# Optimization experiments

Hardware: AMD Instinct MI355X
Metric: run time of the kernel (lower is better)

Reference implementation:

```python
import jax, jax.numpy as jnp
import numpy as np

D_MODEL = 1024
N_HEADS = 16
D_K = D_MODEL // N_HEADS
B, T = 4, 2048


def setup_inputs() -> dict:
    key = jax.random.key(0)
    ks = jax.random.split(key, 13)
    s = 1.0 / np.sqrt(D_MODEL)
    inp = {
        "Q": jax.random.normal(ks[0], (B, T, D_MODEL), jnp.float32),
        "K": jax.random.normal(ks[1], (B, T, D_MODEL), jnp.float32),
        "V": jax.random.normal(ks[2], (B, T, D_MODEL), jnp.float32),
        "mask": jax.random.randint(ks[3], (B, 1, 1, T), 0, 2, jnp.int32),
        "W_q": jax.random.normal(ks[4], (D_MODEL, D_MODEL), jnp.float32) * s,
        "b_q": jax.random.normal(ks[5], (D_MODEL,), jnp.float32) * s,
        "W_k": jax.random.normal(ks[6], (D_MODEL, D_MODEL), jnp.float32) * s,
        "b_k": jax.random.normal(ks[7], (D_MODEL,), jnp.float32) * s,
        "W_v": jax.random.normal(ks[8], (D_MODEL, D_MODEL), jnp.float32) * s,
        "b_v": jax.random.normal(ks[9], (D_MODEL,), jnp.float32) * s,
        "W_o": jax.random.normal(ks[10], (D_MODEL, D_MODEL), jnp.float32) * s,
        "b_o": jax.random.normal(ks[11], (D_MODEL,), jnp.float32) * s,
    }
    return inp


def _split_heads(x):
    # (B, T, d_model) -> (B, H, T, d_k)
    b, t, _ = x.shape
    return x.reshape(b, t, N_HEADS, D_K).transpose(0, 2, 1, 3)


def reference(Q, K, V, mask, W_q, b_q, W_k, b_k, W_v, b_v, W_o, b_o):
    # Linear projections (torch nn.Linear: x @ W.T + b)
    q = _split_heads(Q @ W_q.T + b_q)  # (B, H, T, d_k)
    k = _split_heads(K @ W_k.T + b_k)
    v = _split_heads(V @ W_v.T + b_v)

    scale = 1.0 / jnp.sqrt(jnp.asarray(D_K, q.dtype))
    scores = jnp.einsum('bhqd,bhkd->bhqk', q, k) * scale  # (B, H, T, T)
    scores = jnp.where(mask == 0, -jnp.inf, scores)
    attn = jax.nn.softmax(scores, axis=-1)
    out = jnp.einsum('bhqk,bhkd->bhqd', attn, v)  # (B, H, T, d_k)

    # combine heads: (B, H, T, d_k) -> (B, T, d_model)
    bsz, h, t, dk = out.shape
    out = out.transpose(0, 2, 1, 3).reshape(bsz, t, h * dk)
    return out @ W_o.T + b_o
```

## Files before the change

kernel.cpp:

```cpp
#include <hip/hip_runtime.h>
#include <hip/hip_bf16.h>
#include <stdint.h>

#define NHEADS 16
#define SEQ    2048
#define DMODEL 1024
#define DK     64

#define QB_OFF  0ull
#define KB_OFF  8388608ull
#define VB_OFF  16777216ull
#define WQ_OFF  25165824ull
#define WK_OFF  26214400ull
#define WV_OFF  27262976ull
#define WO_OFF  28311552ull
#define QH_OFF  29360128ull
#define KH_OFF  37748736ull
#define VT_OFF  46137344ull
#define MSKF_OFF 54525952ull
#define OC_OFF  0ull

typedef __attribute__((ext_vector_type(8))) __bf16 bf16x8;
typedef __attribute__((ext_vector_type(4))) float  floatx4;

__device__ __forceinline__ unsigned short f2bf(float f) {
  unsigned int u = __float_as_uint(f);
  u += 0x7fffu + ((u >> 16) & 1u);
  return (unsigned short)(u >> 16);
}

__device__ __forceinline__ void gld_lds16(const void* g, void* l) {
  __builtin_amdgcn_global_load_lds(
      (const __attribute__((address_space(1))) unsigned int*)(g),
      (__attribute__((address_space(3))) unsigned int*)(uintptr_t)(l),
      16, 0, 0);
}

#define WAITVM(N) asm volatile("s_waitcnt vmcnt(" #N ")" ::: "memory")

struct CastArgs {
  const float* src[8];
  unsigned long long off[8];
  unsigned int n[8];
};

__global__ __launch_bounds__(256) void cast_bf16(CastArgs a, unsigned short* __restrict__ ws) {
  int ti = blockIdx.y;
  unsigned int n = a.n[ti];
  unsigned int stride = gridDim.x * blockDim.x * 4u;
  unsigned int i0 = (blockIdx.x * blockDim.x + threadIdx.x) * 4u;
  if (ti == 7) {
    const int* s = (const int*)a.src[7];
    unsigned short* d = ws + a.off[7];
    for (unsigned int i = i0; i < n; i += stride) {
      int4 v = *(const int4*)(s + i);
      ushort4 o;
      o.x = v.x ? 0x3f80u : 0u;
      o.y = v.y ? 0x3f80u : 0u;
      o.z = v.z ? 0x3f80u : 0u;
      o.w = v.w ? 0x3f80u : 0u;
      unsigned int p = (i & ~31u) | ((i & 12u) << 1) | ((i & 16u) >> 2) | (i & 3u);
      *(ushort4*)(d + p) = o;
    }
    return;
  }
  const float* s = a.src[ti];
  unsigned short* d = ws + a.off[ti];
  for (unsigned int i = i0; i < n; i += stride) {
    float4 v = *(const float4*)(s + i);
    ushort4 o;
    o.x = f2bf(v.x); o.y = f2bf(v.y); o.z = f2bf(v.z); o.w = f2bf(v.w);
    *(ushort4*)(d + i) = o;
  }
}

__device__ __forceinline__ void gemm_core_128(
    const unsigned short* __restrict__ A, const unsigned short* __restrict__ Bw,
    int m0, int n0, unsigned short* sm, floatx4 acc[4][4])
{
  int tid = threadIdx.x;
  int lane = tid & 63, l16 = lane & 15, quad = lane >> 4;
  int wave = tid >> 6, wm = wave >> 1, wn = wave & 1;

  #pragma unroll
  for (int rnd = 0; rnd < 2; ++rnd) {
    int e = tid * 8 + rnd * 2048;
    int row = e >> 5, col = e & 31;
    gld_lds16(A  + (size_t)(m0 + row) * 1024 + col, sm + e);
    gld_lds16(Bw + (size_t)(n0 + row) * 1024 + col, sm + 4096 + e);
  }

  int cur = 0;
  #pragma unroll 1
  for (int kt = 0; kt < 31; ++kt) {
    const unsigned short* As = sm + cur * 8192;
    const unsigned short* Bs = As + 4096;

    unsigned short* An = sm + (cur ^ 1) * 8192;
    #pragma unroll
    for (int rnd = 0; rnd < 2; ++rnd) {
      int e = tid * 8 + rnd * 2048;
      int row = e >> 5, col = e & 31;
      gld_lds16(A  + (size_t)(m0 + row) * 1024 + (kt + 1) * 32 + col, An + e);
      gld_lds16(Bw + (size_t)(n0 + row) * 1024 + (kt + 1) * 32 + col, An + 4096 + e);
    }

    WAITVM(4);
    __builtin_amdgcn_s_barrier();
    __builtin_amdgcn_sched_barrier(0);

    bf16x8 af[4], bfr[4];
    #pragma unroll
    for (int f = 0; f < 4; ++f) {
      af[f]  = *(const bf16x8*)(As + (wm * 64 + f * 16 + l16) * 32 + quad * 8);
      bfr[f] = *(const bf16x8*)(Bs + (wn * 64 + f * 16 + l16) * 32 + quad * 8);
    }
    __builtin_amdgcn_s_setprio(1);
    #pragma unroll
    for (int fm = 0; fm < 4; ++fm)
      #pragma unroll
      for (int fn = 0; fn < 4; ++fn)
        acc[fm][fn] = __builtin_amdgcn_mfma_f32_16x16x32_bf16(af[fm], bfr[fn], acc[fm][fn], 0, 0, 0);
    __builtin_amdgcn_s_setprio(0);

    __builtin_amdgcn_s_barrier();
    __builtin_amdgcn_sched_barrier(0);
    cur ^= 1;
  }

  {
    const unsigned short* As = sm + cur * 8192;
    const unsigned short* Bs = As + 4096;
    WAITVM(0);
    __builtin_amdgcn_s_barrier();
    __builtin_amdgcn_sched_barrier(0);
    bf16x8 af[4], bfr[4];
    #pragma unroll
    for (int f = 0; f < 4; ++f) {
      af[f]  = *(const bf16x8*)(As + (wm * 64 + f * 16 + l16) * 32 + quad * 8);
      bfr[f] = *(const bf16x8*)(Bs + (wn * 64 + f * 16 + l16) * 32 + quad * 8);
    }
    #pragma unroll
    for (int fm = 0; fm < 4; ++fm)
      #pragma unroll
      for (int fn = 0; fn < 4; ++fn)
        acc[fm][fn] = __builtin_amdgcn_mfma_f32_16x16x32_bf16(af[fm], bfr[fn], acc[fm][fn], 0, 0, 0);
  }
}

__global__ __launch_bounds__(256) void proj_gemm(
    const unsigned short* __restrict__ wsc, unsigned short* __restrict__ ws,
    const float* __restrict__ bq, const float* __restrict__ bk, const float* __restrict__ bv)
{
  __shared__ unsigned short smem[17408];
  int z = blockIdx.z;
  int tid = threadIdx.x, lane = tid & 63, l16 = lane & 15, quad = lane >> 4;
  int wave = tid >> 6, wm = wave >> 1, wn = wave & 1;

  if (z < 2) {
    const unsigned short* A  = wsc + (z == 0 ? QB_OFF : KB_OFF);
    const unsigned short* Bw = wsc + (z == 0 ? WQ_OFF : WK_OFF);
    const float* bias = (z == 0) ? bq : bk;
    unsigned short* dst = ws + (z == 0 ? QH_OFF : KH_OFF);
    float scale = (z == 0) ? 0.18033688011111772f : 1.0f;

    int flat = blockIdx.y * 8 + blockIdx.x;
    int xcd = flat & 7, slot = flat >> 3;
    int m_t = xcd * 8 + (slot >> 3);
    int n_t = slot & 7;
    int m0 = m_t * 128, n0 = n_t * 128;
    floatx4 acc[4][4] = {};
    gemm_core_128(A, Bw, m0, n0, smem, acc);

    __syncthreads();
    #pragma unroll
    for (int fn = 0; fn < 4; ++fn) {
      int c = wn * 64 + fn * 16 + l16;
      float bvv = bias[n0 + c];
      #pragma unroll
      for (int fm = 0; fm < 4; ++fm)
        #pragma unroll
        for (int r = 0; r < 4; ++r) {
          int t = wm * 64 + fm * 16 + quad * 4 + r;
          smem[t * 136 + c] = f2bf((acc[fm][fn][r] + bvv) * scale);
        }
    }
    __syncthreads();
    #pragma unroll
    for (int it = 0; it < 8; ++it) {
      int e = it * 2048 + tid * 8;
      int t = e >> 7, c = e & 127;
      uint4 val = *(const uint4*)(smem + t * 136 + c);
      int m = m0 + t, b = m >> 11, tg = m & 2047;
      int h = (n0 + c) >> 6, d = (n0 + c) & 63;
      *(uint4*)(dst + ((size_t)(b * NHEADS + h) * SEQ + tg) * DK + d) = val;
    }
  } else {
    int flat = blockIdx.y * 8 + blockIdx.x;
    int b = flat >> 7, rem = flat & 127;
    int mt = rem >> 4, nt = rem & 15;
    int m0 = mt * 128, n0 = nt * 128;
    const unsigned short* A  = wsc + WV_OFF;
    const unsigned short* Bw = wsc + VB_OFF + (size_t)b * SEQ * DMODEL;
    unsigned short* dst = ws + VT_OFF;

    floatx4 acc[4][4] = {};
    gemm_core_128(A, Bw, m0, n0, smem, acc);

    const unsigned short* pm = wsc + MSKF_OFF + (size_t)b * SEQ;
    int tpl[4];
    float mv[4];
    #pragma unroll
    for (int fn = 0; fn < 4; ++fn) {
      int t = wn * 64 + fn * 16 + l16;
      int tp = (t & ~31) | ((t & 12) << 1) | ((t & 16) >> 2) | (t & 3);
      tpl[fn] = tp;
      mv[fn] = __uint_as_float((unsigned int)pm[n0 + tp] << 16);
    }

    __syncthreads();
    #pragma unroll
    for (int fm = 0; fm < 4; ++fm) {
      int mb = m0 + wm * 64 + fm * 16 + quad * 4;
      float4 bb4 = *(const float4*)(bv + mb);
      float bbv[4] = {bb4.x, bb4.y, bb4.z, bb4.w};
      #pragma unroll
      for (int r = 0; r < 4; ++r) {
        int mrow = wm * 64 + fm * 16 + quad * 4 + r;
        #pragma unroll
        for (int fn = 0; fn < 4; ++fn)
          smem[mrow * 136 + tpl[fn]] = f2bf((acc[fm][fn][r] + bbv[r]) * mv[fn]);
      }
    }
    __syncthreads();
    #pragma unroll
    for (int it = 0; it < 8; ++it) {
      int e = it * 2048 + tid * 8;
      int mrow = e >> 7, tcol = e & 127;
      uint4 val = *(const uint4*)(smem + mrow * 136 + tcol);
      int m = m0 + mrow, h = m >> 6, d = m & 63;
      *(uint4*)(dst + ((size_t)(b * NHEADS + h) * DK + d) * SEQ + n0 + tcol) = val;
    }
  }
}

__global__ __launch_bounds__(256, 4) void attn_fused(
    const unsigned short* __restrict__ wsc, unsigned short* __restrict__ ws)
{
  __shared__ unsigned short smem[16640];
  unsigned short* Ks  = smem;
  unsigned short* Vts = smem + 8192;
  unsigned short* MskB = smem + 16384;

  int fid = blockIdx.y * gridDim.x + blockIdx.x;
  int xcd = fid & 7, slot = fid >> 3;
  int bh = xcd * 8 + (slot >> 4);
  int qt = slot & 15;
  int b = bh >> 4, h = bh & 15;
  int tid = threadIdx.x, wave = tid >> 6, lane = tid & 63, l16 = lane & 15, quad = lane >> 4;
  int wq = wave * 32;

  const unsigned short* qh = wsc + QH_OFF + (size_t)bh * SEQ * DK;
  const unsigned short* kh = wsc + KH_OFF + (size_t)bh * SEQ * DK;
  const unsigned short* vt = wsc + VT_OFF + (size_t)bh * DK * SEQ;
  const unsigned short* pm = wsc + MSKF_OFF + (size_t)b * SEQ;

  #pragma unroll
  for (int kk = 0; kk < 2; ++kk)
    #pragma unroll
    for (int rnd = 0; rnd < 2; ++rnd) {
      int e = tid * 8 + rnd * 2048;
      int row = e >> 5, col = e & 31;
      gld_lds16(qh + (size_t)(qt * 128 + row) * DK + kk * 32 + col, Ks + kk * 4096 + e);
    }
  __syncthreads();
  bf16x8 qf[2][2];
  #pragma unroll
  for (int fq = 0; fq < 2; ++fq)
    #pragma unroll
    for (int kk = 0; kk < 2; ++kk)
      qf[fq][kk] = *(const bf16x8*)(Ks + kk * 4096 + (wq + fq * 16 + l16) * 32 + quad * 8);
  __syncthreads();

  #pragma unroll
  for (int kk = 0; kk < 2; ++kk)
    #pragma unroll
    for (int rnd = 0; rnd < 2; ++rnd) {
      int e = tid * 8 + rnd * 2048;
      int row = e >> 5, col = e & 31;
      gld_lds16(kh + (size_t)row * DK + kk * 32 + col, Ks + kk * 4096 + e);
    }
  if (tid < 16)
    gld_lds16(pm + tid * 8, MskB + tid * 8);
  __syncthreads();

  floatx4 o[4][2] = {};
  floatx4 osum[2] = {};
  const floatx4 zero4 = {};

  union PU { unsigned int u[2][4]; bf16x8 v[2]; };

  #pragma unroll 1
  for (int jt = 0; jt < 16; ++jt) {
    #pragma unroll
    for (int kk = 0; kk < 4; ++kk) {
      int e = tid * 8;
      int row = e >> 5, col = e & 31;
      gld_lds16(vt + (size_t)row * SEQ + jt * 128 + kk * 32 + col, Vts + kk * 2048 + e);
    }

    PU pf[4];
    #pragma unroll
    for (int w = 0; w < 4; ++w) {
      floatx4 s[2][2];
      #pragma unroll
      for (int f2 = 0; f2 < 2; ++f2) {
        int fk = 2 * w + f2;
        bf16x8 kf0 = *(const bf16x8*)(Ks +        (fk * 16 + l16) * 32 + quad * 8);
        bf16x8 kf1 = *(const bf16x8*)(Ks + 4096 + (fk * 16 + l16) * 32 + quad * 8);
        #pragma unroll
        for (int fq = 0; fq < 2; ++fq) {
          s[f2][fq] = __builtin_amdgcn_mfma_f32_16x16x32_bf16(kf0, qf[fq][0], zero4, 0, 0, 0);
          s[f2][fq] = __builtin_amdgcn_mfma_f32_16x16x32_bf16(kf1, qf[fq][1], s[f2][fq], 0, 0, 0);
        }
      }
      #pragma unroll
      for (int f2 = 0; f2 < 2; ++f2)
        #pragma unroll
        for (int fq = 0; fq < 2; ++fq)
          #pragma unroll
          for (int r = 0; r < 4; ++r)
            s[f2][fq][r] = __builtin_amdgcn_exp2f(s[f2][fq][r]);

      #pragma unroll
      for (int fq = 0; fq < 2; ++fq) {
        asm("v_cvt_pk_bf16_f32 %0, %1, %2" : "=v"(pf[w].u[fq][0]) : "v"(s[0][fq][0]), "v"(s[0][fq][1]));
        asm("v_cvt_pk_bf16_f32 %0, %1, %2" : "=v"(pf[w].u[fq][1]) : "v"(s[0][fq][2]), "v"(s[0][fq][3]));
        asm("v_cvt_pk_bf16_f32 %0, %1, %2" : "=v"(pf[w].u[fq][2]) : "v"(s[1][fq][0]), "v"(s[1][fq][1]));
        asm("v_cvt_pk_bf16_f32 %0, %1, %2" : "=v"(pf[w].u[fq][3]) : "v"(s[1][fq][2]), "v"(s[1][fq][3]));
      }

      bf16x8 mvf = *(const bf16x8*)(MskB + w * 32 + quad * 8);
      #pragma unroll
      for (int fq = 0; fq < 2; ++fq)
        osum[fq] = __builtin_amdgcn_mfma_f32_16x16x32_bf16(mvf, pf[w].v[fq], osum[fq], 0, 0, 0);
    }

    __syncthreads();

    if (jt < 15) {
      const unsigned short* khn = kh + (size_t)(jt + 1) * 128 * DK;
      #pragma unroll
      for (int kk = 0; kk < 2; ++kk)
        #pragma unroll
        for (int rnd = 0; rnd < 2; ++rnd) {
          int e = tid * 8 + rnd * 2048;
          int row = e >> 5, col = e & 31;
          gld_lds16(khn + (size_t)row * DK + kk * 32 + col, Ks + kk * 4096 + e);
        }
      if (tid < 16)
        gld_lds16(pm + (jt + 1) * 128 + tid * 8, MskB + tid * 8);
    }

    __builtin_amdgcn_s_setprio(1);
    #pragma unroll
    for (int w = 0; w < 4; ++w)
      #pragma unroll
      for (int fd = 0; fd < 4; ++fd) {
        bf16x8 vf = *(const bf16x8*)(Vts + w * 2048 + (fd * 16 + l16) * 32 + quad * 8);
        #pragma unroll
        for (int fq = 0; fq < 2; ++fq)
          o[fd][fq] = __builtin_amdgcn_mfma_f32_16x16x32_bf16(vf, pf[w].v[fq], o[fd][fq], 0, 0, 0);
      }
    __builtin_amdgcn_s_setprio(0);

    __syncthreads();
  }

  float inv[2];
  #pragma unroll
  for (int fq = 0; fq < 2; ++fq)
    inv[fq] = __builtin_amdgcn_rcpf(osum[fq][0]);

  unsigned short* Ot = smem;
  #pragma unroll
  for (int fd = 0; fd < 4; ++fd)
    #pragma unroll
    for (int fq = 0; fq < 2; ++fq)
      #pragma unroll
      for (int r = 0; r < 4; ++r) {
        int q = wq + fq * 16 + l16;
        int d = fd * 16 + quad * 4 + r;
        Ot[q * 72 + d] = f2bf(o[fd][fq][r] * inv[fq]);
      }
  __syncthreads();
  unsigned short* oc = ws + OC_OFF;
  #pragma unroll
  for (int rr = 0; rr < 4; ++rr) {
    int e = rr * 2048 + tid * 8;
    int q = e >> 6, off = e & 63;
    uint4 val = *(const uint4*)(Ot + q * 72 + off);
    *(uint4*)(oc + ((size_t)(b * SEQ + qt * 128 + q)) * DMODEL + h * DK + off) = val;
  }
}

__global__ __launch_bounds__(256) void out_gemm(
    const unsigned short* __restrict__ wsc, const float* __restrict__ bo,
    float* __restrict__ out)
{
  __shared__ unsigned short smem[16384];
  int flat = blockIdx.y * 8 + blockIdx.x;
  int xcd = flat & 7, slot = flat >> 3;
  int m_t = xcd * 8 + (slot >> 3);
  int n_t = slot & 7;
  int m0 = m_t * 128, n0 = n_t * 128;
  floatx4 acc[4][4] = {};
  gemm_core_128(wsc + OC_OFF, wsc + WO_OFF, m0, n0, smem, acc);

  int tid = threadIdx.x, lane = tid & 63, l16 = lane & 15, quad = lane >> 4;
  int wave = tid >> 6, wm = wave >> 1, wn = wave & 1;
  #pragma unroll
  for (int fn = 0; fn < 4; ++fn) {
    int n = n0 + wn * 64 + fn * 16 + l16;
    float bvv = bo[n];
    #pragma unroll
    for (int fm = 0; fm < 4; ++fm)
      #pragma unroll
      for (int r = 0; r < 4; ++r) {
        int m = m0 + wm * 64 + fm * 16 + quad * 4 + r;
        out[(size_t)m * DMODEL + n] = acc[fm][fn][r] + bvv;
      }
  }
}

extern "C" void kernel_launch(void* const* d_in, const int* in_sizes, int n_in,
                              void* d_out, int out_size, void* d_ws, size_t ws_size,
                              hipStream_t stream) {
  const float* Q    = (const float*)d_in[0];
  const float* K    = (const float*)d_in[1];
  const float* V    = (const float*)d_in[2];
  const float* bq   = (const float*)d_in[5];
  const float* bk   = (const float*)d_in[7];
  const float* bv   = (const float*)d_in[9];
  const float* bo   = (const float*)d_in[11];
  unsigned short* ws = (unsigned short*)d_ws;
  float* out = (float*)d_out;

  CastArgs ca;
  ca.src[0] = Q;  ca.src[1] = K;  ca.src[2] = V;
  ca.src[3] = (const float*)d_in[4]; ca.src[4] = (const float*)d_in[6];
  ca.src[5] = (const float*)d_in[8]; ca.src[6] = (const float*)d_in[10];
  ca.src[7] = (const float*)d_in[3];
  ca.off[0] = QB_OFF; ca.off[1] = KB_OFF; ca.off[2] = VB_OFF;
  ca.off[3] = WQ_OFF; ca.off[4] = WK_OFF; ca.off[5] = WV_OFF; ca.off[6] = WO_OFF;
  ca.off[7] = MSKF_OFF;
  ca.n[0] = ca.n[1] = ca.n[2] = 8388608u;
  ca.n[3] = ca.n[4] = ca.n[5] = ca.n[6] = 1048576u;
  ca.n[7] = 8192u;

  hipLaunchKernelGGL(cast_bf16, dim3(2048, 8), dim3(256), 0, stream, ca, ws);
  hipLaunchKernelGGL(proj_gemm, dim3(8, 64, 3), dim3(256), 0, stream, ws, ws, bq, bk, bv);
  hipLaunchKernelGGL(attn_fused, dim3(16, 64), dim3(256), 0, stream, ws, ws);
  hipLaunchKernelGGL(out_gemm, dim3(8, 64), dim3(256), 0, stream, ws, bo, out);
}
```

Measured before the change: 322.6 us.

## Fuse fp32-to-bf16 activation cast into projection GEMM loads

The separate cast pass over the Q, K, V activations is removed. The projection GEMM now reads fp32 activations directly into registers, converts them with packed bf16 convert instructions, and stores them into LDS, which cuts the write and re-read of 48MB of bf16 intermediates. The GEMM core also swaps its manual vmcnt waits and raw barriers for __syncthreads. The fp32 side now goes through registers instead of direct global-to-LDS loads, so it adds register pressure and may expose more load latency per k-tile.

```diff
diff --git a/kernel.cpp b/kernel.cpp
--- a/kernel.cpp
+++ b/kernel.cpp
@@ -8,8 +8,6 @@
 #define DK     64
 
 #define QB_OFF  0ull
-#define KB_OFF  8388608ull
-#define VB_OFF  16777216ull
 #define WQ_OFF  25165824ull
 #define WK_OFF  26214400ull
 #define WV_OFF  27262976ull
@@ -36,12 +34,19 @@
       16, 0, 0);
 }
 
-#define WAITVM(N) asm volatile("s_waitcnt vmcnt(" #N ")" ::: "memory")
+__device__ __forceinline__ uint4 cvt8(const float4& va, const float4& vb) {
+  uint4 w;
+  asm("v_cvt_pk_bf16_f32 %0, %1, %2" : "=v"(w.x) : "v"(va.x), "v"(va.y));
+  asm("v_cvt_pk_bf16_f32 %0, %1, %2" : "=v"(w.y) : "v"(va.z), "v"(va.w));
+  asm("v_cvt_pk_bf16_f32 %0, %1, %2" : "=v"(w.z) : "v"(vb.x), "v"(vb.y));
+  asm("v_cvt_pk_bf16_f32 %0, %1, %2" : "=v"(w.w) : "v"(vb.z), "v"(vb.w));
+  return w;
+}
 
 struct CastArgs {
-  const float* src[8];
-  unsigned long long off[8];
-  unsigned int n[8];
+  const float* src[5];
+  unsigned long long off[5];
+  unsigned int n[5];
 };
 
 __global__ __launch_bounds__(256) void cast_bf16(CastArgs a, unsigned short* __restrict__ ws) {
@@ -49,9 +54,9 @@
   unsigned int n = a.n[ti];
   unsigned int stride = gridDim.x * blockDim.x * 4u;
   unsigned int i0 = (blockIdx.x * blockDim.x + threadIdx.x) * 4u;
-  if (ti == 7) {
-    const int* s = (const int*)a.src[7];
-    unsigned short* d = ws + a.off[7];
+  if (ti == 4) {
+    const int* s = (const int*)a.src[4];
+    unsigned short* d = ws + a.off[4];
     for (unsigned int i = i0; i < n; i += stride) {
       int4 v = *(const int4*)(s + i);
       ushort4 o;
@@ -89,26 +94,23 @@
     gld_lds16(A  + (size_t)(m0 + row) * 1024 + col, sm + e);
     gld_lds16(Bw + (size_t)(n0 + row) * 1024 + col, sm + 4096 + e);
   }
+  __syncthreads();
 
   int cur = 0;
   #pragma unroll 1
-  for (int kt = 0; kt < 31; ++kt) {
+  for (int kt = 0; kt < 32; ++kt) {
     const unsigned short* As = sm + cur * 8192;
     const unsigned short* Bs = As + 4096;
-
-    unsigned short* An = sm + (cur ^ 1) * 8192;
-    #pragma unroll
-    for (int rnd = 0; rnd < 2; ++rnd) {
-      int e = tid * 8 + rnd * 2048;
-      int row = e >> 5, col = e & 31;
-      gld_lds16(A  + (size_t)(m0 + row) * 1024 + (kt + 1) * 32 + col, An + e);
-      gld_lds16(Bw + (size_t)(n0 + row) * 1024 + (kt + 1) * 32 + col, An + 4096 + e);
-    }
-
-    WAITVM(4);
-    __builtin_amdgcn_s_barrier();
-    __builtin_amdgcn_sched_barrier(0);
-
+    if (kt < 31) {
+      unsigned short* An = sm + (cur ^ 1) * 8192;
+      #pragma unroll
+      for (int rnd = 0; rnd < 2; ++rnd) {
+        int e = tid * 8 + rnd * 2048;
+        int row = e >> 5, col = e & 31;
+        gld_lds16(A  + (size_t)(m0 + row) * 1024 + (kt + 1) * 32 + col, An + e);
+        gld_lds16(Bw + (size_t)(n0 + row) * 1024 + (kt + 1) * 32 + col, An + 4096 + e);
+      }
+    }
     bf16x8 af[4], bfr[4];
     #pragma unroll
     for (int f = 0; f < 4; ++f) {
@@ -122,33 +124,87 @@
       for (int fn = 0; fn < 4; ++fn)
         acc[fm][fn] = __builtin_amdgcn_mfma_f32_16x16x32_bf16(af[fm], bfr[fn], acc[fm][fn], 0, 0, 0);
     __builtin_amdgcn_s_setprio(0);
-
-    __builtin_amdgcn_s_barrier();
-    __builtin_amdgcn_sched_barrier(0);
+    __syncthreads();
     cur ^= 1;
   }
-
-  {
+}
+
+template<int F32SIDE>
+__device__ __forceinline__ void gemm_core_128_f32(
+    const float* __restrict__ Fsrc, const unsigned short* __restrict__ Hsrc,
+    int f0, int h0, unsigned short* sm, floatx4 acc[4][4])
+{
+  int tid = threadIdx.x;
+  int lane = tid & 63, l16 = lane & 15, quad = lane >> 4;
+  int wave = tid >> 6, wm = wave >> 1, wn = wave & 1;
+  const int FOFF = (F32SIDE == 0) ? 0 : 4096;
+  const int HOFF = (F32SIDE == 0) ? 4096 : 0;
+
+  #pragma unroll
+  for (int rnd = 0; rnd < 2; ++rnd) {
+    int e = tid * 8 + rnd * 2048;
+    int row = e >> 5, col = e & 31;
+    gld_lds16(Hsrc + (size_t)(h0 + row) * 1024 + col, sm + HOFF + e);
+    const float* p = Fsrc + (size_t)(f0 + row) * 1024 + col;
+    float4 va = *(const float4*)p;
+    float4 vb = *(const float4*)(p + 4);
+    *(uint4*)(sm + FOFF + e) = cvt8(va, vb);
+  }
+  __syncthreads();
+
+  int cur = 0;
+  #pragma unroll 1
+  for (int kt = 0; kt < 32; ++kt) {
     const unsigned short* As = sm + cur * 8192;
     const unsigned short* Bs = As + 4096;
-    WAITVM(0);
-    __builtin_amdgcn_s_barrier();
-    __builtin_amdgcn_sched_barrier(0);
+    unsigned short* nb = sm + (cur ^ 1) * 8192;
+
+    float4 pa0, pb0, pa1, pb1;
+    if (kt < 31) {
+      #pragma unroll
+      for (int rnd = 0; rnd < 2; ++rnd) {
+        int e = tid * 8 + rnd * 2048;
+        int row = e >> 5, col = e & 31;
+        gld_lds16(Hsrc + (size_t)(h0 + row) * 1024 + (kt + 1) * 32 + col, nb + HOFF + e);
+      }
+      {
+        int e = tid * 8;
+        const float* p = Fsrc + (size_t)(f0 + (e >> 5)) * 1024 + (kt + 1) * 32 + (e & 31);
+        pa0 = *(const float4*)p;  pb0 = *(const float4*)(p + 4);
+      }
+      {
+        int e = tid * 8 + 2048;
+        const float* p = Fsrc + (size_t)(f0 + (e >> 5)) * 1024 + (kt + 1) * 32 + (e & 31);
+        pa1 = *(const float4*)p;  pb1 = *(const float4*)(p + 4);
+      }
+    }
+
     bf16x8 af[4], bfr[4];
     #pragma unroll
     for (int f = 0; f < 4; ++f) {
       af[f]  = *(const bf16x8*)(As + (wm * 64 + f * 16 + l16) * 32 + quad * 8);
       bfr[f] = *(const bf16x8*)(Bs + (wn * 64 + f * 16 + l16) * 32 + quad * 8);
     }
+    __builtin_amdgcn_s_setprio(1);
     #pragma unroll
     for (int fm = 0; fm < 4; ++fm)
       #pragma unroll
       for (int fn = 0; fn < 4; ++fn)
         acc[fm][fn] = __builtin_amdgcn_mfma_f32_16x16x32_bf16(af[fm], bfr[fn], acc[fm][fn], 0, 0, 0);
+    __builtin_amdgcn_s_setprio(0);
+
+    if (kt < 31) {
+      *(uint4*)(nb + FOFF + tid * 8)        = cvt8(pa0, pb0);
+      *(uint4*)(nb + FOFF + tid * 8 + 2048) = cvt8(pa1, pb1);
+    }
+    __syncthreads();
+    cur ^= 1;
   }
 }
 
 __global__ __launch_bounds__(256) void proj_gemm(
+    const float* __restrict__ Qf, const float* __restrict__ Kf,
+    const float* __restrict__ Vf,
     const unsigned short* __restrict__ wsc, unsigned short* __restrict__ ws,
     const float* __restrict__ bq, const float* __restrict__ bk, const float* __restrict__ bv)
 {
@@ -158,7 +214,7 @@
   int wave = tid >> 6, wm = wave >> 1, wn = wave & 1;
 
   if (z < 2) {
-    const unsigned short* A  = wsc + (z == 0 ? QB_OFF : KB_OFF);
+    const float* Fa = (z == 0) ? Qf : Kf;
     const unsigned short* Bw = wsc + (z == 0 ? WQ_OFF : WK_OFF);
     const float* bias = (z == 0) ? bq : bk;
     unsigned short* dst = ws + (z == 0 ? QH_OFF : KH_OFF);
@@ -170,7 +226,7 @@
     int n_t = slot & 7;
     int m0 = m_t * 128, n0 = n_t * 128;
     floatx4 acc[4][4] = {};
-    gemm_core_128(A, Bw, m0, n0, smem, acc);
+    gemm_core_128_f32<0>(Fa, Bw, m0, n0, smem, acc);
 
     __syncthreads();
     #pragma unroll
@@ -201,11 +257,11 @@
     int mt = rem >> 4, nt = rem & 15;
     int m0 = mt * 128, n0 = nt * 128;
     const unsigned short* A  = wsc + WV_OFF;
-    const unsigned short* Bw = wsc + VB_OFF + (size_t)b * SEQ * DMODEL;
+    const float* Bf = Vf + (size_t)b * SEQ * DMODEL;
     unsigned short* dst = ws + VT_OFF;
 
     floatx4 acc[4][4] = {};
-    gemm_core_128(A, Bw, m0, n0, smem, acc);
+    gemm_core_128_f32<1>(Bf, A, n0, m0, smem, acc);
 
     const unsigned short* pm = wsc + MSKF_OFF + (size_t)b * SEQ;
     int tpl[4];
@@ -447,19 +503,14 @@
   float* out = (float*)d_out;
 
   CastArgs ca;
-  ca.src[0] = Q;  ca.src[1] = K;  ca.src[2] = V;
-  ca.src[3] = (const float*)d_in[4]; ca.src[4] = (const float*)d_in[6];
-  ca.src[5] = (const float*)d_in[8]; ca.src[6] = (const float*)d_in[10];
-  ca.src[7] = (const float*)d_in[3];
-  ca.off[0] = QB_OFF; ca.off[1] = KB_OFF; ca.off[2] = VB_OFF;
-  ca.off[3] = WQ_OFF; ca.off[4] = WK_OFF; ca.off[5] = WV_OFF; ca.off[6] = WO_OFF;
-  ca.off[7] = MSKF_OFF;
-  ca.n[0] = ca.n[1] = ca.n[2] = 8388608u;
-  ca.n[3] = ca.n[4] = ca.n[5] = ca.n[6] = 1048576u;
-  ca.n[7] = 8192u;
-
-  hipLaunchKernelGGL(cast_bf16, dim3(2048, 8), dim3(256), 0, stream, ca, ws);
-  hipLaunchKernelGGL(proj_gemm, dim3(8, 64, 3), dim3(256), 0, stream, ws, ws, bq, bk, bv);
+  ca.src[0] = (const float*)d_in[4];  ca.off[0] = WQ_OFF;  ca.n[0] = 1048576u;
+  ca.src[1] = (const float*)d_in[6];  ca.off[1] = WK_OFF;  ca.n[1] = 1048576u;
+  ca.src[2] = (const float*)d_in[8];  ca.off[2] = WV_OFF;  ca.n[2] = 1048576u;
+  ca.src[3] = (const float*)d_in[10]; ca.off[3] = WO_OFF;  ca.n[3] = 1048576u;
+  ca.src[4] = (const float*)d_in[3];  ca.off[4] = MSKF_OFF; ca.n[4] = 8192u;
+
+  hipLaunchKernelGGL(cast_bf16, dim3(1024, 5), dim3(256), 0, stream, ca, ws);
+  hipLaunchKernelGGL(proj_gemm, dim3(8, 64, 3), dim3(256), 0, stream, Q, K, V, ws, ws, bq, bk, bv);
   hipLaunchKernelGGL(attn_fused, dim3(16, 64), dim3(256), 0, stream, ws, ws);
   hipLaunchKernelGGL(out_gemm, dim3(8, 64), dim3(256), 0, stream, ws, bo, out);
 }
```

Measured after the change: 333.9 us. +3.5%, slower.
